# Performance work log

Hardware: AMD Instinct MI355X
Metric: run time of the kernel (lower is better)

Reference implementation:

```python
import jax, jax.numpy as jnp
import numpy as np
import math

B, T, D, H = 4, 1024, 512, 8
DH = D // H


def setup_inputs() -> dict:
    key = jax.random.key(0)
    ks = jax.random.split(key, 8)
    s = 1.0 / math.sqrt(D)
    return {
        "x": jax.random.normal(ks[0], (B, T, D), jnp.float32),
        "Wq_w": jax.random.normal(ks[1], (D, D), jnp.float32) * s,
        "Wq_b": jnp.zeros((D,), jnp.float32),
        "Wk_w": jax.random.normal(ks[2], (D, D), jnp.float32) * s,
        "Wk_b": jnp.zeros((D,), jnp.float32),
        "Wv_w": jax.random.normal(ks[3], (D, D), jnp.float32) * s,
        "Wv_b": jnp.zeros((D,), jnp.float32),
        "Ws_w": jax.random.normal(ks[4], (D, H), jnp.float32) * s,
        "Ws_b": jnp.zeros((H,), jnp.float32),
        "Wo_w": jax.random.normal(ks[5], (D, D), jnp.float32) * s,
        "Wo_b": jnp.zeros((D,), jnp.float32),
    }


def reference(x, Wq_w, Wq_b, Wk_w, Wk_b, Wv_w, Wv_b, Ws_w, Ws_b, Wo_w, Wo_b):
    b, t, d = x.shape
    # projections (weights stored [in, out]; same math as torch Linear)
    q = (x @ Wq_w + Wq_b).reshape(b, t, H, DH).transpose(0, 2, 1, 3)  # [B,H,T,dh]
    k = (x @ Wk_w + Wk_b).reshape(b, t, H, DH).transpose(0, 2, 1, 3)
    v = (x @ Wv_w + Wv_b).reshape(b, t, H, DH).transpose(0, 2, 1, 3)

    logits = jnp.einsum("bhtd,bhsd->bhts", q, k) / math.sqrt(DH)
    series = jax.nn.softmax(logits, axis=-1)  # [B,H,T,T] (dropout p=0 -> no-op)

    sigma = jax.nn.softplus(x @ Ws_w + Ws_b).transpose(0, 2, 1) + 1e-6  # [B,H,T]

    idx = jnp.arange(t, dtype=jnp.float32)
    dist2 = (idx[None, :] - idx[:, None]) ** 2  # [T,T]
    s2 = sigma[..., None] ** 2 + 1e-6           # [B,H,T,1]
    prior = jnp.exp(-dist2[None, None] / (2.0 * s2))
    prior = prior / (prior.sum(axis=-1, keepdims=True) + 1e-9)

    out = jnp.einsum("bhts,bhsd->bhtd", series, v)
    out = out.transpose(0, 2, 1, 3).reshape(b, t, d)
    out = out @ Wo_w + Wo_b
    return out, series, prior, sigma
```

## Files before the change

### kernel.cpp

```cpp
#include <hip/hip_runtime.h>
#include <math.h>

#define BB 4
#define TT 1024
#define DD 512
#define HH 8
#define DHH 64

typedef short bf8_t __attribute__((ext_vector_type(8)));
typedef float f32x4 __attribute__((ext_vector_type(4)));

__device__ __forceinline__ float softplus_f(float z) {
    return fmaxf(z, 0.f) + log1pf(__expf(-fabsf(z)));
}

__device__ __forceinline__ unsigned short f2bf(float f) {
    union { float f; unsigned int u; } v; v.f = f;
    return (unsigned short)((v.u + 0x7FFFu + ((v.u >> 16) & 1u)) >> 16);
}

__global__ __launch_bounds__(256) void cast_x_kernel(
    const float* __restrict__ x, unsigned short* __restrict__ xbf)
{
    int i = blockIdx.x * 256 + threadIdx.x;
    float4 a = *(const float4*)&x[(size_t)i * 8];
    float4 b = *(const float4*)&x[(size_t)i * 8 + 4];
    union { unsigned short u[8]; int4 v; } o;
    o.u[0] = f2bf(a.x); o.u[1] = f2bf(a.y); o.u[2] = f2bf(a.z); o.u[3] = f2bf(a.w);
    o.u[4] = f2bf(b.x); o.u[5] = f2bf(b.y); o.u[6] = f2bf(b.z); o.u[7] = f2bf(b.w);
    *(int4*)&xbf[(size_t)i * 8] = o.v;
}

__global__ __launch_bounds__(256) void transpose_w_kernel(
    const float* __restrict__ Wq, const float* __restrict__ Wk,
    const float* __restrict__ Wv, const float* __restrict__ Wo,
    unsigned short* __restrict__ wt, unsigned short* __restrict__ woT)
{
    __shared__ float tile[32][33];
    const int tid = threadIdx.x;
    const int z = blockIdx.z;
    const float* W = (z == 0) ? Wq : (z == 1) ? Wk : (z == 2) ? Wv : Wo;
    unsigned short* dst = (z < 3) ? (wt + (size_t)z * 512 * 512) : woT;
    const int k0 = blockIdx.x * 32, n0 = blockIdx.y * 32;
    const int ty = tid >> 3, tx = tid & 7;

    float4 v = *(const float4*)&W[(size_t)(k0 + ty) * 512 + n0 + tx * 4];
    tile[ty][tx*4+0] = v.x; tile[ty][tx*4+1] = v.y;
    tile[ty][tx*4+2] = v.z; tile[ty][tx*4+3] = v.w;
    __syncthreads();
    ushort4 o;
    o.x = f2bf(tile[tx*4+0][ty]);
    o.y = f2bf(tile[tx*4+1][ty]);
    o.z = f2bf(tile[tx*4+2][ty]);
    o.w = f2bf(tile[tx*4+3][ty]);
    *(ushort4*)&dst[(size_t)(n0 + ty) * 512 + k0 + tx * 4] = o;
}

__global__ __launch_bounds__(256) void transpose_ws_kernel(
    const float* __restrict__ Ws, unsigned short* __restrict__ wt)
{
    const int tid = threadIdx.x;
    #pragma unroll
    for (int i = 0; i < 16; ++i) {
        int idx = i * 256 + tid;
        int k = idx >> 3, n = idx & 7;
        wt[(size_t)(1536 + n) * 512 + k] = f2bf(Ws[idx]);
    }
}

__global__ __launch_bounds__(256) void proj_mfma_kernel(
    const unsigned short* __restrict__ xbf,
    const unsigned short* __restrict__ wt,
    const float* __restrict__ bq, const float* __restrict__ bk,
    const float* __restrict__ bv, const float* __restrict__ bs,
    unsigned short* __restrict__ qbf, unsigned short* __restrict__ kbf,
    unsigned short* __restrict__ vbf, float* __restrict__ sigma_out)
{
    __shared__ unsigned short a_s[64][64];
    __shared__ unsigned short b_s[64][64];
    const int tid = threadIdx.x;
    const int w = tid >> 6, l = tid & 63, lr = l & 15, lg = l >> 4;
    const int ct = blockIdx.x;
    const int m0 = blockIdx.y * 64;
    const int n0 = ct * 64;

    f32x4 acc[4];
    #pragma unroll
    for (int nb = 0; nb < 4; ++nb) acc[nb] = (f32x4){0.f, 0.f, 0.f, 0.f};

    for (int k0 = 0; k0 < 512; k0 += 64) {
        __syncthreads();
        #pragma unroll
        for (int rep = 0; rep < 2; ++rep) {
            int idx = rep * 256 + tid;
            int row = idx >> 3, cg = idx & 7;
            *(int4*)&a_s[row][(cg ^ (row & 7)) * 8] =
                *(const int4*)&xbf[(size_t)(m0 + row) * 512 + k0 + cg * 8];
            *(int4*)&b_s[row][(cg ^ (row & 7)) * 8] =
                *(const int4*)&wt[(size_t)(n0 + row) * 512 + k0 + cg * 8];
        }
        __syncthreads();
        #pragma unroll
        for (int ks = 0; ks < 2; ++ks) {
            int arow = w * 16 + lr;
            bf8_t af = *(const bf8_t*)&a_s[arow][((ks*4 + lg) ^ (arow & 7)) * 8];
            #pragma unroll
            for (int nb = 0; nb < 4; ++nb) {
                int brow = nb * 16 + lr;
                bf8_t bf = *(const bf8_t*)&b_s[brow][((ks*4 + lg) ^ (brow & 7)) * 8];
                acc[nb] = __builtin_amdgcn_mfma_f32_16x16x32_bf16(af, bf, acc[nb], 0, 0, 0);
            }
        }
    }

    if (ct < 24) {
        const int seg = ct >> 3;
        const int h = ct & 7;
        const float* bias = (seg == 0) ? bq : (seg == 1) ? bk : bv;
        unsigned short* dst = (seg == 0) ? qbf : (seg == 1) ? kbf : vbf;
        const float sc = (seg == 0) ? 0.125f : 1.f;
        #pragma unroll
        for (int nb = 0; nb < 4; ++nb) {
            float bb = bias[h * 64 + nb * 16 + lr];
            #pragma unroll
            for (int r = 0; r < 4; ++r) {
                int m = m0 + w * 16 + lg * 4 + r;
                int b = m >> 10, t = m & 1023;
                dst[((size_t)((b*HH + h)*TT + t)) * 64 + nb * 16 + lr] =
                    f2bf((acc[nb][r] + bb) * sc);
            }
        }
    } else if (lr < 8) {
        float bb = bs[lr];
        #pragma unroll
        for (int r = 0; r < 4; ++r) {
            int m = m0 + w * 16 + lg * 4 + r;
            int b = m >> 10, t = m & 1023;
            sigma_out[(size_t)(b*HH + lr)*TT + t] = softplus_f(acc[0][r] + bb) + 1e-6f;
        }
    }
}

__global__ __launch_bounds__(256) void attn_kernel(
    const unsigned short* __restrict__ qbf,
    const unsigned short* __restrict__ kbf,
    const unsigned short* __restrict__ vbf,
    const float* __restrict__ sigma,
    float* __restrict__ series, float* __restrict__ prior,
    unsigned short* __restrict__ obf)
{
    __shared__ unsigned short k_lds[64][72];
    __shared__ unsigned short v_lds[64][64];
    __shared__ unsigned short p_lds[4][16][72];

    const int tid = threadIdx.x;
    const int w  = tid >> 6, l = tid & 63;
    const int lr = l & 15,  lg = l >> 4;
    const int bh = blockIdx.y;
    const int qr = blockIdx.x * 64 + w * 16;

    bf8_t aq[2];
    {
        const unsigned short* qrow = &qbf[((size_t)bh * TT + qr + lr) * 64];
        aq[0] = *(const bf8_t*)&qrow[lg * 8];
        aq[1] = *(const bf8_t*)&qrow[32 + lg * 8];
    }

    float psum[4] = {0.f, 0.f, 0.f, 0.f};
    for (int st = 0; st < 16; ++st) {
        __syncthreads();
        #pragma unroll
        for (int rep = 0; rep < 2; ++rep) {
            int idx = rep * 256 + tid;
            int tr = idx >> 3, cg = idx & 7;
            *(int4*)&k_lds[tr][cg * 8] =
                *(const int4*)&kbf[((size_t)bh * TT + st * 64 + tr) * 64 + cg * 8];
        }
        __syncthreads();
        #pragma unroll
        for (int nb = 0; nb < 4; ++nb) {
            f32x4 acc = {0.f, 0.f, 0.f, 0.f};
            #pragma unroll
            for (int c = 0; c < 2; ++c) {
                bf8_t bk = *(const bf8_t*)&k_lds[nb * 16 + lr][c * 32 + lg * 8];
                acc = __builtin_amdgcn_mfma_f32_16x16x32_bf16(aq[c], bk, acc, 0, 0, 0);
            }
            #pragma unroll
            for (int r = 0; r < 4; ++r) psum[r] += __expf(acc[r]);
        }
    }
    #pragma unroll
    for (int r = 0; r < 4; ++r) {
        psum[r] += __shfl_xor(psum[r], 1);
        psum[r] += __shfl_xor(psum[r], 2);
        psum[r] += __shfl_xor(psum[r], 4);
        psum[r] += __shfl_xor(psum[r], 8);
    }
    float inv[4];
    #pragma unroll
    for (int r = 0; r < 4; ++r) inv[r] = 1.f / psum[r];

    f32x4 oacc[4];
    #pragma unroll
    for (int nb = 0; nb < 4; ++nb) oacc[nb] = (f32x4){0.f, 0.f, 0.f, 0.f};

    for (int st = 0; st < 16; ++st) {
        __syncthreads();
        #pragma unroll
        for (int rep = 0; rep < 2; ++rep) {
            int idx = rep * 256 + tid;
            int tr = idx >> 3, cg = idx & 7;
            *(int4*)&k_lds[tr][cg * 8] =
                *(const int4*)&kbf[((size_t)bh * TT + st * 64 + tr) * 64 + cg * 8];
        }
        #pragma unroll
        for (int rep = 0; rep < 2; ++rep) {
            int idx = rep * 256 + tid;
            int sr = idx >> 3, cg = idx & 7;
            int4 vv = *(const int4*)&vbf[((size_t)bh * TT + st * 64 + sr) * 64 + cg * 8];
            const unsigned short* pv = (const unsigned short*)&vv;
            #pragma unroll
            for (int j = 0; j < 8; ++j) {
                int row = cg * 8 + j;
                int gsw = ((sr >> 3) ^ j ^ cg) & 7;
                v_lds[row][gsw * 8 + (sr & 7)] = pv[j];
            }
        }
        __syncthreads();

        #pragma unroll
        for (int nb = 0; nb < 4; ++nb) {
            f32x4 acc = {0.f, 0.f, 0.f, 0.f};
            #pragma unroll
            for (int c = 0; c < 2; ++c) {
                bf8_t bk = *(const bf8_t*)&k_lds[nb * 16 + lr][c * 32 + lg * 8];
                acc = __builtin_amdgcn_mfma_f32_16x16x32_bf16(aq[c], bk, acc, 0, 0, 0);
            }
            #pragma unroll
            for (int r = 0; r < 4; ++r) {
                float e = __expf(acc[r]);
                series[((size_t)bh * TT + qr + lg * 4 + r) * TT + st * 64 + nb * 16 + lr]
                    = e * inv[r];
                p_lds[w][lg * 4 + r][nb * 16 + lr] = f2bf(e);
            }
        }

        bf8_t pa0 = *(const bf8_t*)&p_lds[w][lr][lg * 8];
        bf8_t pa1 = *(const bf8_t*)&p_lds[w][lr][32 + lg * 8];
        #pragma unroll
        for (int nb = 0; nb < 4; ++nb) {
            #pragma unroll
            for (int c = 0; c < 2; ++c) {
                int row = nb * 16 + lr;
                int gsw = ((c * 4 + lg) ^ (row & 7) ^ (row >> 3)) & 7;
                bf8_t bv = *(const bf8_t*)&v_lds[row][gsw * 8];
                oacc[nb] = __builtin_amdgcn_mfma_f32_16x16x32_bf16(
                    (c == 0) ? pa0 : pa1, bv, oacc[nb], 0, 0, 0);
            }
        }

        {
            int t = qr + st;
            float sg = sigma[(size_t)bh * TT + t];
            float cc = 1.f / (2.f * (sg * sg + 1e-6f));
            float e[16]; float sum = 0.f;
            #pragma unroll
            for (int j = 0; j < 16; ++j) {
                float d = (float)(t - (j * 64 + l));
                e[j] = __expf(-(d * d) * cc);
                sum += e[j];
            }
            sum += __shfl_xor(sum, 32);
            sum += __shfl_xor(sum, 16);
            sum += __shfl_xor(sum, 8);
            sum += __shfl_xor(sum, 4);
            sum += __shfl_xor(sum, 2);
            sum += __shfl_xor(sum, 1);
            float pinv = 1.f / (sum + 1e-9f);
            float* pr = prior + ((size_t)bh * TT + t) * TT;
            #pragma unroll
            for (int j = 0; j < 16; ++j) pr[j * 64 + l] = e[j] * pinv;
        }
    }

    const int b = bh >> 3, h = bh & 7;
    #pragma unroll
    for (int nb = 0; nb < 4; ++nb)
        #pragma unroll
        for (int r = 0; r < 4; ++r) {
            int t = qr + lg * 4 + r;
            obf[((size_t)(b * TT + t)) * 512 + h * 64 + nb * 16 + lr] =
                f2bf(oacc[nb][r] * inv[r]);
        }
}

__global__ __launch_bounds__(256) void outproj_mfma_kernel(
    const unsigned short* __restrict__ obf,
    const unsigned short* __restrict__ woT,
    const float* __restrict__ bo, float* __restrict__ out)
{
    __shared__ unsigned short a_s[64][64];
    __shared__ unsigned short b_s[64][64];
    const int tid = threadIdx.x;
    const int w = tid >> 6, l = tid & 63, lr = l & 15, lg = l >> 4;
    const int n0 = blockIdx.x * 64;
    const int m0 = blockIdx.y * 64;

    f32x4 acc[4];
    #pragma unroll
    for (int nb = 0; nb < 4; ++nb) acc[nb] = (f32x4){0.f, 0.f, 0.f, 0.f};

    for (int k0 = 0; k0 < 512; k0 += 64) {
        __syncthreads();
        #pragma unroll
        for (int rep = 0; rep < 2; ++rep) {
            int idx = rep * 256 + tid;
            int row = idx >> 3, cg = idx & 7;
            *(int4*)&a_s[row][(cg ^ (row & 7)) * 8] =
                *(const int4*)&obf[(size_t)(m0 + row) * 512 + k0 + cg * 8];
            *(int4*)&b_s[row][(cg ^ (row & 7)) * 8] =
                *(const int4*)&woT[(size_t)(n0 + row) * 512 + k0 + cg * 8];
        }
        __syncthreads();
        #pragma unroll
        for (int ks = 0; ks < 2; ++ks) {
            int arow = w * 16 + lr;
            bf8_t af = *(const bf8_t*)&a_s[arow][((ks*4 + lg) ^ (arow & 7)) * 8];
            #pragma unroll
            for (int nb = 0; nb < 4; ++nb) {
                int brow = nb * 16 + lr;
                bf8_t bf = *(const bf8_t*)&b_s[brow][((ks*4 + lg) ^ (brow & 7)) * 8];
                acc[nb] = __builtin_amdgcn_mfma_f32_16x16x32_bf16(af, bf, acc[nb], 0, 0, 0);
            }
        }
    }

    #pragma unroll
    for (int nb = 0; nb < 4; ++nb) {
        float bb = bo[n0 + nb * 16 + lr];
        #pragma unroll
        for (int r = 0; r < 4; ++r) {
            int m = m0 + w * 16 + lg * 4 + r;
            out[(size_t)m * 512 + n0 + nb * 16 + lr] = acc[nb][r] + bb;
        }
    }
}

extern "C" void kernel_launch(void* const* d_in, const int* in_sizes, int n_in,
                              void* d_out, int out_size, void* d_ws, size_t ws_size,
                              hipStream_t stream)
{
    const float* x    = (const float*)d_in[0];
    const float* Wq_w = (const float*)d_in[1];
    const float* Wq_b = (const float*)d_in[2];
    const float* Wk_w = (const float*)d_in[3];
    const float* Wk_b = (const float*)d_in[4];
    const float* Wv_w = (const float*)d_in[5];
    const float* Wv_b = (const float*)d_in[6];
    const float* Ws_w = (const float*)d_in[7];
    const float* Ws_b = (const float*)d_in[8];
    const float* Wo_w = (const float*)d_in[9];
    const float* Wo_b = (const float*)d_in[10];

    float* out    = (float*)d_out;
    float* series = out + (size_t)BB*TT*DD;
    float* prior  = series + (size_t)BB*HH*TT*TT;
    float* sigma  = prior + (size_t)BB*HH*TT*TT;

    const size_t nx = (size_t)BB*TT*DD;
    unsigned short* xbf = (unsigned short*)d_ws;
    unsigned short* wt  = xbf + nx;
    unsigned short* woT = wt + (size_t)1600*512;
    unsigned short* qbf = woT + (size_t)512*512;
    unsigned short* kbf = qbf + nx;
    unsigned short* vbf = kbf + nx;
    unsigned short* obf = vbf + nx;

    cast_x_kernel<<<1024, 256, 0, stream>>>(x, xbf);
    transpose_w_kernel<<<dim3(16, 16, 4), 256, 0, stream>>>(
        Wq_w, Wk_w, Wv_w, Wo_w, wt, woT);
    transpose_ws_kernel<<<1, 256, 0, stream>>>(Ws_w, wt);

    proj_mfma_kernel<<<dim3(25, 64), 256, 0, stream>>>(
        xbf, wt, Wq_b, Wk_b, Wv_b, Ws_b, qbf, kbf, vbf, sigma);

    attn_kernel<<<dim3(16, 32), 256, 0, stream>>>(
        qbf, kbf, vbf, sigma, series, prior, obf);

    outproj_mfma_kernel<<<dim3(8, 64), 256, 0, stream>>>(obf, woT, Wo_b, out);
}
```

Baseline: 117.6 us.

## Read K/V directly from global via pre-transposed V, drop LDS staging and syncs

Adds a separate kernel that transposes V into a [bh, dh, T] layout. The attention kernel can then load K and V fragments straight from global/L2 into MFMA operands, with no LDS staging and no per-tile __syncthreads. The prior computation moves out of the main loop into a tail loop that writes contiguous float4 stores per lane instead of strided scalar stores. The Ws transpose is folded into the weight-transpose launch, removing one kernel launch. In exchange it adds an extra pass over V and relies on cache hits for K/V fragments that each wave now re-reads from global.

```diff
diff --git a/kernel.cpp b/kernel.cpp
--- a/kernel.cpp
+++ b/kernel.cpp
@@ -34,11 +34,22 @@
 __global__ __launch_bounds__(256) void transpose_w_kernel(
     const float* __restrict__ Wq, const float* __restrict__ Wk,
     const float* __restrict__ Wv, const float* __restrict__ Wo,
+    const float* __restrict__ Ws,
     unsigned short* __restrict__ wt, unsigned short* __restrict__ woT)
 {
     __shared__ float tile[32][33];
     const int tid = threadIdx.x;
     const int z = blockIdx.z;
+    if (z == 4) {
+        if (blockIdx.x != 0 || blockIdx.y != 0) return;
+        #pragma unroll
+        for (int i = 0; i < 16; ++i) {
+            int idx = i * 256 + tid;
+            int k = idx >> 3, n = idx & 7;
+            wt[(size_t)(1536 + n) * 512 + k] = f2bf(Ws[idx]);
+        }
+        return;
+    }
     const float* W = (z == 0) ? Wq : (z == 1) ? Wk : (z == 2) ? Wv : Wo;
     unsigned short* dst = (z < 3) ? (wt + (size_t)z * 512 * 512) : woT;
     const int k0 = blockIdx.x * 32, n0 = blockIdx.y * 32;
@@ -56,15 +67,30 @@
     *(ushort4*)&dst[(size_t)(n0 + ty) * 512 + k0 + tx * 4] = o;
 }
 
-__global__ __launch_bounds__(256) void transpose_ws_kernel(
-    const float* __restrict__ Ws, unsigned short* __restrict__ wt)
-{
-    const int tid = threadIdx.x;
-    #pragma unroll
-    for (int i = 0; i < 16; ++i) {
-        int idx = i * 256 + tid;
-        int k = idx >> 3, n = idx & 7;
-        wt[(size_t)(1536 + n) * 512 + k] = f2bf(Ws[idx]);
+__global__ __launch_bounds__(256) void transpose_v_kernel(
+    const unsigned short* __restrict__ vbf, unsigned short* __restrict__ vT)
+{
+    __shared__ unsigned short t_s[64][72];
+    const int tid = threadIdx.x;
+    const int bh = blockIdx.y;
+    const int s0 = blockIdx.x * 64;
+
+    #pragma unroll
+    for (int rep = 0; rep < 2; ++rep) {
+        int idx = rep * 256 + tid;
+        int sr = idx >> 3, cg = idx & 7;
+        int4 vv = *(const int4*)&vbf[((size_t)bh * TT + s0 + sr) * 64 + cg * 8];
+        const unsigned short* pv = (const unsigned short*)&vv;
+        #pragma unroll
+        for (int j = 0; j < 8; ++j) t_s[cg * 8 + j][sr] = pv[j];
+    }
+    __syncthreads();
+    #pragma unroll
+    for (int rep = 0; rep < 2; ++rep) {
+        int idx = rep * 256 + tid;
+        int dh = idx >> 3, cg = idx & 7;
+        *(int4*)&vT[((size_t)bh * 64 + dh) * TT + s0 + cg * 8] =
+            *(const int4*)&t_s[dh][cg * 8];
     }
 }
 
@@ -144,13 +170,11 @@
 __global__ __launch_bounds__(256) void attn_kernel(
     const unsigned short* __restrict__ qbf,
     const unsigned short* __restrict__ kbf,
-    const unsigned short* __restrict__ vbf,
+    const unsigned short* __restrict__ vT,
     const float* __restrict__ sigma,
     float* __restrict__ series, float* __restrict__ prior,
     unsigned short* __restrict__ obf)
 {
-    __shared__ unsigned short k_lds[64][72];
-    __shared__ unsigned short v_lds[64][64];
     __shared__ unsigned short p_lds[4][16][72];
 
     const int tid = threadIdx.x;
@@ -158,6 +182,9 @@
     const int lr = l & 15,  lg = l >> 4;
     const int bh = blockIdx.y;
     const int qr = blockIdx.x * 64 + w * 16;
+
+    const unsigned short* kb = kbf + (size_t)bh * TT * 64;
+    const unsigned short* vb = vT  + (size_t)bh * 64 * TT;
 
     bf8_t aq[2];
     {
@@ -168,21 +195,12 @@
 
     float psum[4] = {0.f, 0.f, 0.f, 0.f};
     for (int st = 0; st < 16; ++st) {
-        __syncthreads();
-        #pragma unroll
-        for (int rep = 0; rep < 2; ++rep) {
-            int idx = rep * 256 + tid;
-            int tr = idx >> 3, cg = idx & 7;
-            *(int4*)&k_lds[tr][cg * 8] =
-                *(const int4*)&kbf[((size_t)bh * TT + st * 64 + tr) * 64 + cg * 8];
-        }
-        __syncthreads();
         #pragma unroll
         for (int nb = 0; nb < 4; ++nb) {
             f32x4 acc = {0.f, 0.f, 0.f, 0.f};
             #pragma unroll
             for (int c = 0; c < 2; ++c) {
-                bf8_t bk = *(const bf8_t*)&k_lds[nb * 16 + lr][c * 32 + lg * 8];
+                bf8_t bk = *(const bf8_t*)&kb[(size_t)(st*64 + nb*16 + lr)*64 + c*32 + lg*8];
                 acc = __builtin_amdgcn_mfma_f32_16x16x32_bf16(aq[c], bk, acc, 0, 0, 0);
             }
             #pragma unroll
@@ -205,35 +223,12 @@
     for (int nb = 0; nb < 4; ++nb) oacc[nb] = (f32x4){0.f, 0.f, 0.f, 0.f};
 
     for (int st = 0; st < 16; ++st) {
-        __syncthreads();
-        #pragma unroll
-        for (int rep = 0; rep < 2; ++rep) {
-            int idx = rep * 256 + tid;
-            int tr = idx >> 3, cg = idx & 7;
-            *(int4*)&k_lds[tr][cg * 8] =
-                *(const int4*)&kbf[((size_t)bh * TT + st * 64 + tr) * 64 + cg * 8];
-        }
-        #pragma unroll
-        for (int rep = 0; rep < 2; ++rep) {
-            int idx = rep * 256 + tid;
-            int sr = idx >> 3, cg = idx & 7;
-            int4 vv = *(const int4*)&vbf[((size_t)bh * TT + st * 64 + sr) * 64 + cg * 8];
-            const unsigned short* pv = (const unsigned short*)&vv;
-            #pragma unroll
-            for (int j = 0; j < 8; ++j) {
-                int row = cg * 8 + j;
-                int gsw = ((sr >> 3) ^ j ^ cg) & 7;
-                v_lds[row][gsw * 8 + (sr & 7)] = pv[j];
-            }
-        }
-        __syncthreads();
-
         #pragma unroll
         for (int nb = 0; nb < 4; ++nb) {
             f32x4 acc = {0.f, 0.f, 0.f, 0.f};
             #pragma unroll
             for (int c = 0; c < 2; ++c) {
-                bf8_t bk = *(const bf8_t*)&k_lds[nb * 16 + lr][c * 32 + lg * 8];
+                bf8_t bk = *(const bf8_t*)&kb[(size_t)(st*64 + nb*16 + lr)*64 + c*32 + lg*8];
                 acc = __builtin_amdgcn_mfma_f32_16x16x32_bf16(aq[c], bk, acc, 0, 0, 0);
             }
             #pragma unroll
@@ -251,35 +246,10 @@
         for (int nb = 0; nb < 4; ++nb) {
             #pragma unroll
             for (int c = 0; c < 2; ++c) {
-                int row = nb * 16 + lr;
-                int gsw = ((c * 4 + lg) ^ (row & 7) ^ (row >> 3)) & 7;
-                bf8_t bv = *(const bf8_t*)&v_lds[row][gsw * 8];
+                bf8_t bv = *(const bf8_t*)&vb[(size_t)(nb*16 + lr)*TT + st*64 + c*32 + lg*8];
                 oacc[nb] = __builtin_amdgcn_mfma_f32_16x16x32_bf16(
                     (c == 0) ? pa0 : pa1, bv, oacc[nb], 0, 0, 0);
             }
-        }
-
-        {
-            int t = qr + st;
-            float sg = sigma[(size_t)bh * TT + t];
-            float cc = 1.f / (2.f * (sg * sg + 1e-6f));
-            float e[16]; float sum = 0.f;
-            #pragma unroll
-            for (int j = 0; j < 16; ++j) {
-                float d = (float)(t - (j * 64 + l));
-                e[j] = __expf(-(d * d) * cc);
-                sum += e[j];
-            }
-            sum += __shfl_xor(sum, 32);
-            sum += __shfl_xor(sum, 16);
-            sum += __shfl_xor(sum, 8);
-            sum += __shfl_xor(sum, 4);
-            sum += __shfl_xor(sum, 2);
-            sum += __shfl_xor(sum, 1);
-            float pinv = 1.f / (sum + 1e-9f);
-            float* pr = prior + ((size_t)bh * TT + t) * TT;
-            #pragma unroll
-            for (int j = 0; j < 16; ++j) pr[j * 64 + l] = e[j] * pinv;
         }
     }
 
@@ -292,6 +262,34 @@
             obf[((size_t)(b * TT + t)) * 512 + h * 64 + nb * 16 + lr] =
                 f2bf(oacc[nb][r] * inv[r]);
         }
+
+    for (int rr = 0; rr < 16; ++rr) {
+        int t = qr + rr;
+        float sg = sigma[(size_t)bh * TT + t];
+        float cc = 1.f / (2.f * (sg * sg + 1e-6f));
+        float e[16]; float sum = 0.f;
+        #pragma unroll
+        for (int j = 0; j < 16; ++j) {
+            float d = (float)(t - (l * 16 + j));
+            e[j] = __expf(-(d * d) * cc);
+            sum += e[j];
+        }
+        sum += __shfl_xor(sum, 32);
+        sum += __shfl_xor(sum, 16);
+        sum += __shfl_xor(sum, 8);
+        sum += __shfl_xor(sum, 4);
+        sum += __shfl_xor(sum, 2);
+        sum += __shfl_xor(sum, 1);
+        float pinv = 1.f / (sum + 1e-9f);
+        float* pr = prior + ((size_t)bh * TT + t) * TT + l * 16;
+        #pragma unroll
+        for (int g = 0; g < 4; ++g) {
+            float4 o;
+            o.x = e[g*4+0] * pinv; o.y = e[g*4+1] * pinv;
+            o.z = e[g*4+2] * pinv; o.w = e[g*4+3] * pinv;
+            *(float4*)&pr[g * 4] = o;
+        }
+    }
 }
 
 __global__ __launch_bounds__(256) void outproj_mfma_kernel(
@@ -374,18 +372,20 @@
     unsigned short* qbf = woT + (size_t)512*512;
     unsigned short* kbf = qbf + nx;
     unsigned short* vbf = kbf + nx;
-    unsigned short* obf = vbf + nx;
+    unsigned short* vTb = vbf + nx;
+    unsigned short* obf = vTb + nx;
 
     cast_x_kernel<<<1024, 256, 0, stream>>>(x, xbf);
-    transpose_w_kernel<<<dim3(16, 16, 4), 256, 0, stream>>>(
-        Wq_w, Wk_w, Wv_w, Wo_w, wt, woT);
-    transpose_ws_kernel<<<1, 256, 0, stream>>>(Ws_w, wt);
+    transpose_w_kernel<<<dim3(16, 16, 5), 256, 0, stream>>>(
+        Wq_w, Wk_w, Wv_w, Wo_w, Ws_w, wt, woT);
 
     proj_mfma_kernel<<<dim3(25, 64), 256, 0, stream>>>(
         xbf, wt, Wq_b, Wk_b, Wv_b, Ws_b, qbf, kbf, vbf, sigma);
 
+    transpose_v_kernel<<<dim3(16, 32), 256, 0, stream>>>(vbf, vTb);
+
     attn_kernel<<<dim3(16, 32), 256, 0, stream>>>(
-        qbf, kbf, vbf, sigma, series, prior, obf);
+        qbf, kbf, vTb, sigma, series, prior, obf);
 
     outproj_mfma_kernel<<<dim3(8, 64), 256, 0, stream>>>(obf, woT, Wo_b, out);
 }
```

Measured after the change: 193.3 us. 1.64x slower.

## Double-buffer K/V tiles in attention kernel and fold Ws transpose into weight transpose

Applied to the files above, without the earlier changes.

The attention kernel now double-buffers the K and V shared-memory tiles. The next tile is prefetched into registers while the current tile is computed, then written to the alternate buffer, so each iteration needs one barrier instead of two. The separate Ws transpose kernel is merged into the weight transpose launch as an extra z-slice, removing one kernel launch. This doubles K/V LDS usage and adds register pressure from the prefetch registers. The kernel is dominated by writing the series and prior outputs to memory, which may limit any benefit.

```diff
diff --git a/kernel.cpp b/kernel.cpp
--- a/kernel.cpp
+++ b/kernel.cpp
@@ -17,6 +17,11 @@
 __device__ __forceinline__ unsigned short f2bf(float f) {
     union { float f; unsigned int u; } v; v.f = f;
     return (unsigned short)((v.u + 0x7FFFu + ((v.u >> 16) & 1u)) >> 16);
+}
+
+__device__ __forceinline__ void bar_lgkm() {
+    asm volatile("s_waitcnt lgkmcnt(0)" ::: "memory");
+    __builtin_amdgcn_s_barrier();
 }
 
 __global__ __launch_bounds__(256) void cast_x_kernel(
@@ -34,11 +39,22 @@
 __global__ __launch_bounds__(256) void transpose_w_kernel(
     const float* __restrict__ Wq, const float* __restrict__ Wk,
     const float* __restrict__ Wv, const float* __restrict__ Wo,
+    const float* __restrict__ Ws,
     unsigned short* __restrict__ wt, unsigned short* __restrict__ woT)
 {
     __shared__ float tile[32][33];
     const int tid = threadIdx.x;
     const int z = blockIdx.z;
+    if (z == 4) {
+        if (blockIdx.x != 0 || blockIdx.y != 0) return;
+        #pragma unroll
+        for (int i = 0; i < 16; ++i) {
+            int idx = i * 256 + tid;
+            int k = idx >> 3, n = idx & 7;
+            wt[(size_t)(1536 + n) * 512 + k] = f2bf(Ws[idx]);
+        }
+        return;
+    }
     const float* W = (z == 0) ? Wq : (z == 1) ? Wk : (z == 2) ? Wv : Wo;
     unsigned short* dst = (z < 3) ? (wt + (size_t)z * 512 * 512) : woT;
     const int k0 = blockIdx.x * 32, n0 = blockIdx.y * 32;
@@ -56,18 +72,6 @@
     *(ushort4*)&dst[(size_t)(n0 + ty) * 512 + k0 + tx * 4] = o;
 }
 
-__global__ __launch_bounds__(256) void transpose_ws_kernel(
-    const float* __restrict__ Ws, unsigned short* __restrict__ wt)
-{
-    const int tid = threadIdx.x;
-    #pragma unroll
-    for (int i = 0; i < 16; ++i) {
-        int idx = i * 256 + tid;
-        int k = idx >> 3, n = idx & 7;
-        wt[(size_t)(1536 + n) * 512 + k] = f2bf(Ws[idx]);
-    }
-}
-
 __global__ __launch_bounds__(256) void proj_mfma_kernel(
     const unsigned short* __restrict__ xbf,
     const unsigned short* __restrict__ wt,
@@ -149,8 +153,8 @@
     float* __restrict__ series, float* __restrict__ prior,
     unsigned short* __restrict__ obf)
 {
-    __shared__ unsigned short k_lds[64][72];
-    __shared__ unsigned short v_lds[64][64];
+    __shared__ unsigned short k_lds[2][64][72];
+    __shared__ unsigned short v_lds[2][64][64];
     __shared__ unsigned short p_lds[4][16][72];
 
     const int tid = threadIdx.x;
@@ -159,6 +163,10 @@
     const int bh = blockIdx.y;
     const int qr = blockIdx.x * 64 + w * 16;
 
+    const int srow = tid >> 3, scg = tid & 7;
+    const unsigned short* kb = kbf + (size_t)bh * TT * 64;
+    const unsigned short* vb = vbf + (size_t)bh * TT * 64;
+
     bf8_t aq[2];
     {
         const unsigned short* qrow = &qbf[((size_t)bh * TT + qr + lr) * 64];
@@ -166,27 +174,36 @@
         aq[1] = *(const bf8_t*)&qrow[32 + lg * 8];
     }
 
+    int4 kreg0, kreg1, vreg0, vreg1;
+
     float psum[4] = {0.f, 0.f, 0.f, 0.f};
+    kreg0 = *(const int4*)&kb[(size_t)srow * 64 + scg * 8];
+    kreg1 = *(const int4*)&kb[(size_t)(32 + srow) * 64 + scg * 8];
+    *(int4*)&k_lds[0][srow][scg * 8] = kreg0;
+    *(int4*)&k_lds[0][32 + srow][scg * 8] = kreg1;
+    bar_lgkm();
+
     for (int st = 0; st < 16; ++st) {
-        __syncthreads();
-        #pragma unroll
-        for (int rep = 0; rep < 2; ++rep) {
-            int idx = rep * 256 + tid;
-            int tr = idx >> 3, cg = idx & 7;
-            *(int4*)&k_lds[tr][cg * 8] =
-                *(const int4*)&kbf[((size_t)bh * TT + st * 64 + tr) * 64 + cg * 8];
-        }
-        __syncthreads();
+        const int cur = st & 1;
+        if (st < 15) {
+            kreg0 = *(const int4*)&kb[(size_t)((st+1)*64 + srow) * 64 + scg * 8];
+            kreg1 = *(const int4*)&kb[(size_t)((st+1)*64 + 32 + srow) * 64 + scg * 8];
+        }
         #pragma unroll
         for (int nb = 0; nb < 4; ++nb) {
             f32x4 acc = {0.f, 0.f, 0.f, 0.f};
             #pragma unroll
             for (int c = 0; c < 2; ++c) {
-                bf8_t bk = *(const bf8_t*)&k_lds[nb * 16 + lr][c * 32 + lg * 8];
+                bf8_t bk = *(const bf8_t*)&k_lds[cur][nb * 16 + lr][c * 32 + lg * 8];
                 acc = __builtin_amdgcn_mfma_f32_16x16x32_bf16(aq[c], bk, acc, 0, 0, 0);
             }
             #pragma unroll
             for (int r = 0; r < 4; ++r) psum[r] += __expf(acc[r]);
+        }
+        if (st < 15) {
+            *(int4*)&k_lds[cur ^ 1][srow][scg * 8] = kreg0;
+            *(int4*)&k_lds[cur ^ 1][32 + srow][scg * 8] = kreg1;
+            bar_lgkm();
         }
     }
     #pragma unroll
@@ -204,36 +221,41 @@
     #pragma unroll
     for (int nb = 0; nb < 4; ++nb) oacc[nb] = (f32x4){0.f, 0.f, 0.f, 0.f};
 
+    kreg0 = *(const int4*)&kb[(size_t)srow * 64 + scg * 8];
+    kreg1 = *(const int4*)&kb[(size_t)(32 + srow) * 64 + scg * 8];
+    vreg0 = *(const int4*)&vb[(size_t)srow * 64 + scg * 8];
+    vreg1 = *(const int4*)&vb[(size_t)(32 + srow) * 64 + scg * 8];
+    *(int4*)&k_lds[0][srow][scg * 8] = kreg0;
+    *(int4*)&k_lds[0][32 + srow][scg * 8] = kreg1;
+    {
+        const unsigned short* pv0 = (const unsigned short*)&vreg0;
+        const unsigned short* pv1 = (const unsigned short*)&vreg1;
+        #pragma unroll
+        for (int j = 0; j < 8; ++j) {
+            int row = scg * 8 + j;
+            int g0 = ((srow >> 3) ^ j ^ scg) & 7;
+            int g1 = ((srow >> 3) ^ 4 ^ j ^ scg) & 7;
+            v_lds[0][row][g0 * 8 + (srow & 7)] = pv0[j];
+            v_lds[0][row][g1 * 8 + (srow & 7)] = pv1[j];
+        }
+    }
+    bar_lgkm();
+
     for (int st = 0; st < 16; ++st) {
-        __syncthreads();
-        #pragma unroll
-        for (int rep = 0; rep < 2; ++rep) {
-            int idx = rep * 256 + tid;
-            int tr = idx >> 3, cg = idx & 7;
-            *(int4*)&k_lds[tr][cg * 8] =
-                *(const int4*)&kbf[((size_t)bh * TT + st * 64 + tr) * 64 + cg * 8];
-        }
-        #pragma unroll
-        for (int rep = 0; rep < 2; ++rep) {
-            int idx = rep * 256 + tid;
-            int sr = idx >> 3, cg = idx & 7;
-            int4 vv = *(const int4*)&vbf[((size_t)bh * TT + st * 64 + sr) * 64 + cg * 8];
-            const unsigned short* pv = (const unsigned short*)&vv;
-            #pragma unroll
-            for (int j = 0; j < 8; ++j) {
-                int row = cg * 8 + j;
-                int gsw = ((sr >> 3) ^ j ^ cg) & 7;
-                v_lds[row][gsw * 8 + (sr & 7)] = pv[j];
-            }
-        }
-        __syncthreads();
+        const int cur = st & 1;
+        if (st < 15) {
+            kreg0 = *(const int4*)&kb[(size_t)((st+1)*64 + srow) * 64 + scg * 8];
+            kreg1 = *(const int4*)&kb[(size_t)((st+1)*64 + 32 + srow) * 64 + scg * 8];
+            vreg0 = *(const int4*)&vb[(size_t)((st+1)*64 + srow) * 64 + scg * 8];
+            vreg1 = *(const int4*)&vb[(size_t)((st+1)*64 + 32 + srow) * 64 + scg * 8];
+        }
 
         #pragma unroll
         for (int nb = 0; nb < 4; ++nb) {
             f32x4 acc = {0.f, 0.f, 0.f, 0.f};
             #pragma unroll
             for (int c = 0; c < 2; ++c) {
-                bf8_t bk = *(const bf8_t*)&k_lds[nb * 16 + lr][c * 32 + lg * 8];
+                bf8_t bk = *(const bf8_t*)&k_lds[cur][nb * 16 + lr][c * 32 + lg * 8];
                 acc = __builtin_amdgcn_mfma_f32_16x16x32_bf16(aq[c], bk, acc, 0, 0, 0);
             }
             #pragma unroll
@@ -253,7 +275,7 @@
             for (int c = 0; c < 2; ++c) {
                 int row = nb * 16 + lr;
                 int gsw = ((c * 4 + lg) ^ (row & 7) ^ (row >> 3)) & 7;
-                bf8_t bv = *(const bf8_t*)&v_lds[row][gsw * 8];
+                bf8_t bv = *(const bf8_t*)&v_lds[cur][row][gsw * 8];
                 oacc[nb] = __builtin_amdgcn_mfma_f32_16x16x32_bf16(
                     (c == 0) ? pa0 : pa1, bv, oacc[nb], 0, 0, 0);
             }
@@ -280,6 +302,22 @@
             float* pr = prior + ((size_t)bh * TT + t) * TT;
             #pragma unroll
             for (int j = 0; j < 16; ++j) pr[j * 64 + l] = e[j] * pinv;
+        }
+
+        if (st < 15) {
+            *(int4*)&k_lds[cur ^ 1][srow][scg * 8] = kreg0;
+            *(int4*)&k_lds[cur ^ 1][32 + srow][scg * 8] = kreg1;
+            const unsigned short* pv0 = (const unsigned short*)&vreg0;
+            const unsigned short* pv1 = (const unsigned short*)&vreg1;
+            #pragma unroll
+            for (int j = 0; j < 8; ++j) {
+                int row = scg * 8 + j;
+                int g0 = ((srow >> 3) ^ j ^ scg) & 7;
+                int g1 = ((srow >> 3) ^ 4 ^ j ^ scg) & 7;
+                v_lds[cur ^ 1][row][g0 * 8 + (srow & 7)] = pv0[j];
+                v_lds[cur ^ 1][row][g1 * 8 + (srow & 7)] = pv1[j];
+            }
+            bar_lgkm();
         }
     }
 
@@ -377,9 +415,8 @@
     unsigned short* obf = vbf + nx;
 
     cast_x_kernel<<<1024, 256, 0, stream>>>(x, xbf);
-    transpose_w_kernel<<<dim3(16, 16, 4), 256, 0, stream>>>(
-        Wq_w, Wk_w, Wv_w, Wo_w, wt, woT);
-    transpose_ws_kernel<<<1, 256, 0, stream>>>(Ws_w, wt);
+    transpose_w_kernel<<<dim3(16, 16, 5), 256, 0, stream>>>(
+        Wq_w, Wk_w, Wv_w, Wo_w, Ws_w, wt, woT);
 
     proj_mfma_kernel<<<dim3(25, 64), 256, 0, stream>>>(
         xbf, wt, Wq_b, Wk_b, Wv_b, Ws_b, qbf, kbf, vbf, sigma);
```

Result: faster. 105.4 us (-10.3%).
